# Optimization experiments

Measured on AMD Instinct MI355X. Metric: run time of the kernel, lower is better.

Reference implementation:

```python
import jax, jax.numpy as jnp
import numpy as np

# coefficients for v1..v24 in the summed expression:
# v1:1, v2-v6:2, v7:1, v8-v12:2, v13:1, v14-v18:2, v19-v24:1
COEFFS = np.ones(24, dtype=np.float32)
COEFFS[1:6] = 2.0   # v2..v6
COEFFS[7:12] = 2.0  # v8..v12
COEFFS[13:18] = 2.0 # v14..v18

B, CIN, L = 16, 16, 8192
NBR, COUT, K = 24, 64, 3

def setup_inputs() -> dict:
    key = jax.random.key(0)
    k1, k2, k3 = jax.random.split(key, 3)
    fan_in = CIN * K
    bound = 1.0 / np.sqrt(fan_in)
    x1 = jax.random.normal(k1, (B, CIN, L), dtype=jnp.float32)
    W = jax.random.uniform(k2, (NBR, COUT, CIN, K), minval=-bound, maxval=bound, dtype=jnp.float32)
    b = jax.random.uniform(k3, (NBR, COUT), minval=-bound, maxval=bound, dtype=jnp.float32)
    return {"x1": x1, "W": W, "b": b}

def reference(x1, W, b):
    c = jnp.asarray(COEFFS)
    # single conv over all 24 branches stacked into out channels
    w_all = W.reshape(NBR * COUT, CIN, K)  # [24*64, 16, 3]
    y = jax.lax.conv_general_dilated(
        x1, w_all, window_strides=(1,), padding=[(1, 1)],
        dimension_numbers=("NCH", "OIH", "NCH"))  # [B, 24*64, L]
    y = y.reshape(x1.shape[0], NBR, COUT, L) + b[None, :, :, None]
    v25 = jnp.einsum("bkcl,k->bcl", y, c)
    return jax.nn.relu(v25)
```

## Files before the change

kernel.cpp:

```cpp
#include <hip/hip_runtime.h>

#define NBR   24
#define CIN   16
#define COUT  64
#define LEN   8192
#define BATCH 16
#define KW    3

#define TL      256
#define NC      8
#define THREADS 512

#define NW (COUT * CIN * KW)

typedef float v2f __attribute__((ext_vector_type(2)));

__device__ __constant__ float d_coef[NBR] = {1,2,2,2,2,2, 1,2,2,2,2,2,
                                             1,2,2,2,2,2, 1,1,1,1,1,1};

static __device__ __forceinline__ v2f fma2(v2f x, float s, v2f c) {
    v2f r;
    r.x = fmaf(x.x, s, c.x);
    r.y = fmaf(x.y, s, c.y);
    return r;
}

__global__ void prep_fold(const float* __restrict__ W, const float* __restrict__ b,
                          float* __restrict__ Weff, float* __restrict__ beff) {
    int idx = blockIdx.x * blockDim.x + threadIdx.x;
    if (idx < NW) {
        float s = 0.f;
#pragma unroll
        for (int k = 0; k < NBR; ++k)
            s += d_coef[k] * W[k * NW + idx];
        int t  = idx % KW;
        int ci = (idx / KW) % CIN;
        int c  = idx / (KW * CIN);
        Weff[(ci * COUT + c) * KW + t] = s;
    } else if (idx < NW + COUT) {
        int c = idx - NW;
        float s = 0.f;
#pragma unroll
        for (int k = 0; k < NBR; ++k)
            s += d_coef[k] * b[k * COUT + c];
        beff[c] = s;
    }
}

__global__ __launch_bounds__(THREADS) void conv_fused(
        const float* __restrict__ x, const float* __restrict__ Weff,
        const float* __restrict__ beff, float* __restrict__ out) {
    __shared__ float xs[CIN][TL + 4];

    const int tid  = threadIdx.x;
    const int blk  = blockIdx.x;
    const int b    = blk >> 5;
    const int tile = blk & 31;
    const int gl0  = tile * TL;

    const float* xb = x + (size_t)b * CIN * LEN;

    for (int idx = tid; idx < CIN * (TL + 2); idx += THREADS) {
        int ci = idx / (TL + 2);
        int j  = idx - ci * (TL + 2);
        int gl = gl0 - 1 + j;
        xs[ci][j] = (gl >= 0 && gl < LEN) ? xb[ci * LEN + gl] : 0.f;
    }
    __syncthreads();

    const int wave = __builtin_amdgcn_readfirstlane(tid >> 6);
    const int lane = tid & 63;
    const int c0   = wave * NC;
    const int l0   = lane * 4;

    v2f A[NC][2];
#pragma unroll
    for (int c = 0; c < NC; ++c) {
        float bv = beff[c0 + c];
        A[c][0].x = bv; A[c][0].y = bv;
        A[c][1].x = bv; A[c][1].y = bv;
    }

    const float* wbase = Weff + c0 * KW;
#pragma unroll
    for (int ci = 0; ci < CIN; ++ci) {
        float4 xa  = *reinterpret_cast<const float4*>(&xs[ci][l0]);
        float2 xb2 = *reinterpret_cast<const float2*>(&xs[ci][l0 + 4]);
        v2f P01, P12, P23, P34, P45;
        P01.x = xa.x;  P01.y = xa.y;
        P12.x = xa.y;  P12.y = xa.z;
        P23.x = xa.z;  P23.y = xa.w;
        P34.x = xa.w;  P34.y = xb2.x;
        P45.x = xb2.x; P45.y = xb2.y;
        const float* wci = wbase + ci * COUT * KW;
#pragma unroll
        for (int c = 0; c < NC; ++c) {
            float w0 = wci[c * KW + 0];
            float w1 = wci[c * KW + 1];
            float w2 = wci[c * KW + 2];
            A[c][0] = fma2(P01, w0, fma2(P12, w1, fma2(P23, w2, A[c][0])));
            A[c][1] = fma2(P23, w0, fma2(P34, w1, fma2(P45, w2, A[c][1])));
        }
    }

    float* ob = out + (size_t)b * COUT * LEN + gl0 + l0;
#pragma unroll
    for (int c = 0; c < NC; ++c) {
        float4 r;
        r.x = fmaxf(A[c][0].x, 0.f);
        r.y = fmaxf(A[c][0].y, 0.f);
        r.z = fmaxf(A[c][1].x, 0.f);
        r.w = fmaxf(A[c][1].y, 0.f);
        *reinterpret_cast<float4*>(ob + (size_t)(c0 + c) * LEN) = r;
    }
}

extern "C" void kernel_launch(void* const* d_in, const int* in_sizes, int n_in,
                              void* d_out, int out_size, void* d_ws, size_t ws_size,
                              hipStream_t stream) {
    const float* x = (const float*)d_in[0];
    const float* W = (const float*)d_in[1];
    const float* b = (const float*)d_in[2];
    float* out = (float*)d_out;

    float* Weff = (float*)d_ws;
    float* beff = Weff + NW;
    const int prep_n = NW + COUT;
    prep_fold<<<(prep_n + 255) / 256, 256, 0, stream>>>(W, b, Weff, beff);
    conv_fused<<<BATCH * (LEN / TL), THREADS, 0, stream>>>(x, Weff, beff, out);
}
```

Baseline: 85.72 us.

## Fuse branch weight folding into conv kernel, staging folded weights in LDS

Drops the separate prep kernel and folds the 24 weighted branch weights and biases inside every conv block, writing them to shared memory. The inner loop then reads per-wave weights as float4 LDS loads instead of global/scalar loads. This removes one kernel launch and the workspace round trip. In exchange every one of the 512 blocks redundantly reads the full 24x3072 weight tensor (about 295KB per block, mostly served from L2) and does the 24-term reduction itself.

```diff
diff --git a/kernel.cpp b/kernel.cpp
--- a/kernel.cpp
+++ b/kernel.cpp
@@ -25,10 +25,22 @@
     return r;
 }
 
-__global__ void prep_fold(const float* __restrict__ W, const float* __restrict__ b,
-                          float* __restrict__ Weff, float* __restrict__ beff) {
-    int idx = blockIdx.x * blockDim.x + threadIdx.x;
-    if (idx < NW) {
+__global__ __launch_bounds__(THREADS) void conv_all(
+        const float* __restrict__ x, const float* __restrict__ W,
+        const float* __restrict__ bias, float* __restrict__ out) {
+    __shared__ float xs[CIN][TL + 4];
+    __shared__ float wf[NW];
+    __shared__ float bf[COUT];
+
+    const int tid  = threadIdx.x;
+    const int blk  = blockIdx.x;
+    const int b    = blk >> 5;
+    const int tile = blk & 31;
+    const int gl0  = tile * TL;
+
+#pragma unroll
+    for (int it = 0; it < NW / THREADS; ++it) {
+        int idx = it * THREADS + tid;
         float s = 0.f;
 #pragma unroll
         for (int k = 0; k < NBR; ++k)
@@ -36,30 +48,17 @@
         int t  = idx % KW;
         int ci = (idx / KW) % CIN;
         int c  = idx / (KW * CIN);
-        Weff[(ci * COUT + c) * KW + t] = s;
-    } else if (idx < NW + COUT) {
-        int c = idx - NW;
+        wf[(ci * COUT + c) * KW + t] = s;
+    }
+    if (tid < COUT) {
         float s = 0.f;
 #pragma unroll
         for (int k = 0; k < NBR; ++k)
-            s += d_coef[k] * b[k * COUT + c];
-        beff[c] = s;
+            s += d_coef[k] * bias[k * COUT + tid];
+        bf[tid] = s;
     }
-}
-
-__global__ __launch_bounds__(THREADS) void conv_fused(
-        const float* __restrict__ x, const float* __restrict__ Weff,
-        const float* __restrict__ beff, float* __restrict__ out) {
-    __shared__ float xs[CIN][TL + 4];
-
-    const int tid  = threadIdx.x;
-    const int blk  = blockIdx.x;
-    const int b    = blk >> 5;
-    const int tile = blk & 31;
-    const int gl0  = tile * TL;
 
     const float* xb = x + (size_t)b * CIN * LEN;
-
     for (int idx = tid; idx < CIN * (TL + 2); idx += THREADS) {
         int ci = idx / (TL + 2);
         int j  = idx - ci * (TL + 2);
@@ -76,12 +75,11 @@
     v2f A[NC][2];
 #pragma unroll
     for (int c = 0; c < NC; ++c) {
-        float bv = beff[c0 + c];
+        float bv = bf[c0 + c];
         A[c][0].x = bv; A[c][0].y = bv;
         A[c][1].x = bv; A[c][1].y = bv;
     }
 
-    const float* wbase = Weff + c0 * KW;
 #pragma unroll
     for (int ci = 0; ci < CIN; ++ci) {
         float4 xa  = *reinterpret_cast<const float4*>(&xs[ci][l0]);
@@ -92,12 +90,21 @@
         P23.x = xa.z;  P23.y = xa.w;
         P34.x = xa.w;  P34.y = xb2.x;
         P45.x = xb2.x; P45.y = xb2.y;
-        const float* wci = wbase + ci * COUT * KW;
+
+        const float4* wq = reinterpret_cast<const float4*>(&wf[(ci * COUT + c0) * KW]);
+        float4 wv0 = wq[0], wv1 = wq[1], wv2 = wq[2];
+        float4 wv3 = wq[3], wv4 = wq[4], wv5 = wq[5];
+        float wreg[24] = {wv0.x, wv0.y, wv0.z, wv0.w,
+                          wv1.x, wv1.y, wv1.z, wv1.w,
+                          wv2.x, wv2.y, wv2.z, wv2.w,
+                          wv3.x, wv3.y, wv3.z, wv3.w,
+                          wv4.x, wv4.y, wv4.z, wv4.w,
+                          wv5.x, wv5.y, wv5.z, wv5.w};
 #pragma unroll
         for (int c = 0; c < NC; ++c) {
-            float w0 = wci[c * KW + 0];
-            float w1 = wci[c * KW + 1];
-            float w2 = wci[c * KW + 2];
+            float w0 = wreg[c * KW + 0];
+            float w1 = wreg[c * KW + 1];
+            float w2 = wreg[c * KW + 2];
             A[c][0] = fma2(P01, w0, fma2(P12, w1, fma2(P23, w2, A[c][0])));
             A[c][1] = fma2(P23, w0, fma2(P34, w1, fma2(P45, w2, A[c][1])));
         }
@@ -123,9 +130,5 @@
     const float* b = (const float*)d_in[2];
     float* out = (float*)d_out;
 
-    float* Weff = (float*)d_ws;
-    float* beff = Weff + NW;
-    const int prep_n = NW + COUT;
-    prep_fold<<<(prep_n + 255) / 256, 256, 0, stream>>>(W, b, Weff, beff);
-    conv_fused<<<BATCH * (LEN / TL), THREADS, 0, stream>>>(x, Weff, beff, out);
+    conv_all<<<BATCH * (LEN / TL), THREADS, 0, stream>>>(x, W, b, out);
 }
```

Result: no change. 84.10 us (-1.9%).
